# Optimization experiments

Measured on AMD Instinct MI355X. Metric: run time of the kernel, lower is better.

The kernel has to match this reference:

```python
import jax, jax.numpy as jnp
import numpy as np

B = 512       # number of graphs
MAX_N = 128   # pad length (>= max(num_atoms))
D = 256       # emb_dim


def setup_inputs() -> dict:
    key = jax.random.key(0)
    ks = jax.random.split(key, 20)
    num_atoms_np = np.full(B, 80, dtype=np.int64)
    num_atoms_np[: B // 2] = 112
    num_atoms_np[B // 2 :] = 48
    total = int(num_atoms_np.sum())  # 40960, static
    scale = 1.0 / np.sqrt(D)

    def lin_w(k):
        return jax.random.normal(k, (D, D), jnp.float32) * scale

    inp = {
        'rep_2d': jax.random.normal(ks[0], (total, D), jnp.float32),
        'rep_3d': jax.random.normal(ks[1], (total, D), jnp.float32),
        'num_atoms': jnp.asarray(num_atoms_np),
        # mha_2d_3d (queries from 2d, keys/values from 3d)
        'wq23': lin_w(ks[2]), 'bq23': jnp.zeros((D,), jnp.float32),
        'wk23': lin_w(ks[3]), 'bk23': jnp.zeros((D,), jnp.float32),
        'wv23': lin_w(ks[4]), 'bv23': jnp.zeros((D,), jnp.float32),
        # mha_3d_2d (queries from 3d, keys/values from 2d)
        'wq32': lin_w(ks[5]), 'bq32': jnp.zeros((D,), jnp.float32),
        'wk32': lin_w(ks[6]), 'bk32': jnp.zeros((D,), jnp.float32),
        'wv32': lin_w(ks[7]), 'bv32': jnp.zeros((D,), jnp.float32),
        # per-branch Linear (normalizer=Identity) + GELU
        'wm23': lin_w(ks[8]), 'bm23': jnp.zeros((D,), jnp.float32),
        'wm32': lin_w(ks[9]), 'bm32': jnp.zeros((D,), jnp.float32),
    }
    return inp


def _variadic_to_padded(flat, num_atoms):
    # flat: [total, D] -> padded [B, MAX_N, D], mask [B, MAX_N] (True = valid)
    cum = jnp.cumsum(num_atoms)
    offsets = cum - num_atoms
    pos = jnp.arange(MAX_N)
    mask = pos[None, :] < num_atoms[:, None]
    idx = jnp.where(mask, offsets[:, None] + pos[None, :], 0)
    padded = flat[idx] * mask[..., None].astype(flat.dtype)
    return padded, mask


def _padded_to_variadic(padded, num_atoms, total):
    # padded: [B, MAX_N, D] -> flat [total, D]
    cum = jnp.cumsum(num_atoms)
    t = jnp.arange(total)
    b = jnp.searchsorted(cum, t, side='right')
    i = t - (cum - num_atoms)[b]
    return padded[b, i]


def _cross_attn(q_in, kv_in, mask, wq, bq, wk, bk, wv, bv):
    # single-head scaled dot-product cross-attention, key-side padding mask
    q = q_in @ wq.T + bq
    k = kv_in @ wk.T + bk
    v = kv_in @ wv.T + bv
    s = jnp.einsum('bqd,bkd->bqk', q, k) / jnp.sqrt(jnp.asarray(D, q.dtype))
    s = jnp.where(mask[:, None, :], s, jnp.asarray(-1e9, s.dtype))
    a = jax.nn.softmax(s, axis=-1)
    return jnp.einsum('bqk,bkd->bqd', a, v)


def reference(rep_2d, rep_3d, num_atoms,
              wq23, bq23, wk23, bk23, wv23, bv23,
              wq32, bq32, wk32, bk32, wv32, bv32,
              wm23, bm23, wm32, bm32):
    total = rep_2d.shape[0]
    p2d, mask = _variadic_to_padded(rep_2d, num_atoms)
    p3d, _ = _variadic_to_padded(rep_3d, num_atoms)
    x2d = _cross_attn(p2d, p3d, mask, wq23, bq23, wk23, bk23, wv23, bv23)
    x3d = _cross_attn(p3d, p2d, mask, wq32, bq32, wk32, bk32, wv32, bv32)
    x2d = _padded_to_variadic(x2d, num_atoms, total)
    x3d = _padded_to_variadic(x3d, num_atoms, total)
    out2d = jax.nn.gelu(x2d @ wm23.T + bm23, approximate=False)
    out3d = jax.nn.gelu(x3d @ wm32.T + bm32, approximate=False)
    return (out2d, out3d)
```

## Files before the change

### kernel.cpp

```cpp
#include <hip/hip_runtime.h>
#include <hip/hip_bf16.h>
#include <cstdint>


typedef short s16x8 __attribute__((ext_vector_type(8)));
typedef float f32x4 __attribute__((ext_vector_type(4)));

__device__ __forceinline__ s16x8 cvt8(const float* p) {
  float4 a0 = *(const float4*)p, a1 = *(const float4*)(p + 4);
  union { s16x8 v; __bf16 e[8]; } u;
  u.e[0] = (__bf16)a0.x; u.e[1] = (__bf16)a0.y; u.e[2] = (__bf16)a0.z; u.e[3] = (__bf16)a0.w;
  u.e[4] = (__bf16)a1.x; u.e[5] = (__bf16)a1.y; u.e[6] = (__bf16)a1.z; u.e[7] = (__bf16)a1.w;
  return u.v;
}
__device__ __forceinline__ float fast_gelu(float x) {
  float ax = fabsf(x);
  float t = 1.0f / (1.0f + 0.3275911f * (ax * 0.70710678f));
  float y = t * (0.254829592f + t * (-0.284496736f + t * (1.421413741f +
            t * (-1.453152027f + t * 1.061405429f))));
  float er = 1.0f - y * __expf(-0.5f * ax * ax);
  er = (x < 0.f) ? -er : er;
  return 0.5f * x * (1.0f + er);
}

__global__ void sentinel_kernel(float* out, float v) {
  if (threadIdx.x == 0 && blockIdx.x == 0) out[0] = v;
}

__global__ __launch_bounds__(512) void scan_kernel(
    const int* __restrict__ na, int* __restrict__ offs,
    int B, int total, float* out)
{
  __shared__ int s32[512];
  __shared__ int s64[512];
  const int t = threadIdx.x;
  int v32 = 0, v64 = 0;
  if (t < B) {
    v32 = na[t];
    v64 = (int)((const long long*)na)[t];
  }
  s32[t] = v32; s64[t] = v64;
  __syncthreads();
  for (int o = 1; o < 512; o <<= 1) {
    int a = (t >= o) ? s32[t - o] : 0;
    int b = (t >= o) ? s64[t - o] : 0;
    __syncthreads();
    s32[t] += a; s64[t] += b;
    __syncthreads();
  }
  int tot32 = s32[B - 1], tot64 = s64[B - 1];
  bool ok32 = (tot32 == total), ok64 = (tot64 == total);
  if (t < B) offs[t] = ok32 ? (s32[t] - v32) : ok64 ? (s64[t] - v64) : 0;
  if (t == 0) {
    offs[B] = ok32 ? tot32 : ok64 ? tot64 : 0;
    if (!ok32 && !ok64) out[0] = 31337.0f;
  }
}

__global__ __launch_bounds__(256) void cvt2_kernel(
    const float* __restrict__ in0, const float* __restrict__ in1,
    __bf16* __restrict__ out0, __bf16* __restrict__ out1) {
  const float* in = blockIdx.y ? in1 : in0;
  __bf16* out = blockIdx.y ? out1 : out0;
  int i = (blockIdx.x * 256 + threadIdx.x) * 4;
  float4 f = *(const float4*)(in + i);
  out[i + 0] = (__bf16)f.x; out[i + 1] = (__bf16)f.y;
  out[i + 2] = (__bf16)f.z; out[i + 3] = (__bf16)f.w;
}

__global__ __launch_bounds__(256) void gemm_kernel(
    const float* __restrict__ A, const float* __restrict__ Bw,
    const float* __restrict__ bias, __bf16* __restrict__ C, int N)
{
  __shared__ __bf16 At[128 * 32];
  __shared__ __bf16 Bt[128 * 32];
  const int t = threadIdx.x;
  const int lane = t & 63, w = t >> 6;
  const int wr = w >> 1, wc = w & 1;
  const int l15 = lane & 15, l4 = lane >> 4;
  const int by = blockIdx.x, bx = blockIdx.y;

  f32x4 acc[4][4];
  for (int m = 0; m < 4; ++m)
    for (int nn = 0; nn < 4; ++nn) acc[m][nn] = (f32x4){0.f, 0.f, 0.f, 0.f};

  for (int kk = 0; kk < 256; kk += 32) {
    for (int j = 0; j < 2; ++j) {
      int c = t + j * 256;
      int row = c >> 2, off0 = (c & 3) * 8;
      *(s16x8*)(&At[row * 32 + off0]) = cvt8(A + (size_t)(by * 128 + row) * 256 + kk + off0);
      *(s16x8*)(&Bt[row * 32 + off0]) = cvt8(Bw + (size_t)(bx * 128 + row) * 256 + kk + off0);
    }
    __syncthreads();
    s16x8 af[4], bfr[4];
    for (int m = 0; m < 4; ++m)
      af[m] = *(const s16x8*)(&At[(wr * 64 + m * 16 + l15) * 32 + l4 * 8]);
    for (int nn = 0; nn < 4; ++nn)
      bfr[nn] = *(const s16x8*)(&Bt[(wc * 64 + nn * 16 + l15) * 32 + l4 * 8]);
    for (int m = 0; m < 4; ++m)
      for (int nn = 0; nn < 4; ++nn)
        acc[m][nn] = __builtin_amdgcn_mfma_f32_16x16x32_bf16(af[m], bfr[nn], acc[m][nn], 0, 0, 0);
    __syncthreads();
  }

  for (int m = 0; m < 4; ++m) {
    int row0 = by * 128 + wr * 64 + m * 16 + l4 * 4;
    for (int nn = 0; nn < 4; ++nn) {
      int col = bx * 128 + wc * 64 + nn * 16 + l15;
      float bc = bias[col];
      for (int r = 0; r < 4; ++r) {
        int row = row0 + r;
        C[(size_t)row * N + col] = (__bf16)(acc[m][nn][r] + bc);
      }
    }
  }
}

#define CTP 136
__global__ __launch_bounds__(256) void vgemm_kernel(
    const float* __restrict__ A, const float* __restrict__ Bw,
    const float* __restrict__ bias, __bf16* __restrict__ Vt, int total)
{
  __shared__ __bf16 At[128 * 32];
  __shared__ __bf16 Bt[128 * 32];
  __shared__ __bf16 Ct[128 * CTP];
  const int t = threadIdx.x;
  const int lane = t & 63, w = t >> 6;
  const int wr = w >> 1, wc = w & 1;
  const int l15 = lane & 15, l4 = lane >> 4;
  const int by = blockIdx.x, bx = blockIdx.y;

  f32x4 acc[4][4];
  for (int m = 0; m < 4; ++m)
    for (int nn = 0; nn < 4; ++nn) acc[m][nn] = (f32x4){0.f, 0.f, 0.f, 0.f};

  for (int kk = 0; kk < 256; kk += 32) {
    for (int j = 0; j < 2; ++j) {
      int c = t + j * 256;
      int row = c >> 2, off0 = (c & 3) * 8;
      *(s16x8*)(&At[row * 32 + off0]) = cvt8(A + (size_t)(by * 128 + row) * 256 + kk + off0);
      *(s16x8*)(&Bt[row * 32 + off0]) = cvt8(Bw + (size_t)(bx * 128 + row) * 256 + kk + off0);
    }
    __syncthreads();
    s16x8 af[4], bfr[4];
    for (int m = 0; m < 4; ++m)
      af[m] = *(const s16x8*)(&At[(wr * 64 + m * 16 + l15) * 32 + l4 * 8]);
    for (int nn = 0; nn < 4; ++nn)
      bfr[nn] = *(const s16x8*)(&Bt[(wc * 64 + nn * 16 + l15) * 32 + l4 * 8]);
    for (int m = 0; m < 4; ++m)
      for (int nn = 0; nn < 4; ++nn)
        acc[m][nn] = __builtin_amdgcn_mfma_f32_16x16x32_bf16(af[m], bfr[nn], acc[m][nn], 0, 0, 0);
    __syncthreads();
  }

  for (int m = 0; m < 4; ++m) {
    int rl0 = wr * 64 + m * 16 + l4 * 4;
    for (int nn = 0; nn < 4; ++nn) {
      int cl = wc * 64 + nn * 16 + l15;
      for (int r = 0; r < 4; ++r) {
        int rl = rl0 + r;
        Ct[rl * CTP + cl] = (__bf16)(acc[m][nn][r] + bias[by * 128 + rl]);
      }
    }
  }
  __syncthreads();

  for (int i = 0; i < 8; ++i) {
    int c = t + i * 256;
    int row = c >> 4, seg = c & 15;
    *(uint4*)(Vt + (size_t)(by * 128 + row) * total + bx * 128 + seg * 8) =
        *(const uint4*)(&Ct[row * CTP + seg * 8]);
  }
}

struct Attn2Args {
  const __bf16* Q[2]; const __bf16* K[2]; const __bf16* V[2];
  unsigned long long X[2];
};
#define KP 264
#define PP 136
#define XP 272
__global__ __launch_bounds__(512, 2) void attn2_kernel(
    Attn2Args args, const int* __restrict__ offs, int total)
{
  __shared__ __bf16 smem[128 * 136];
  __bf16 (*Klds)[KP] = (__bf16(*)[KP])smem;
  __bf16 (*Plds)[PP] = (__bf16(*)[PP])smem;
  __bf16 (*XT)[XP]   = (__bf16(*)[XP])smem;

  const int br = blockIdx.y;
  const __bf16* Q  = args.Q[br];
  const __bf16* Km = args.K[br];
  const __bf16* Vt = args.V[br];
  __bf16* X = (__bf16*)args.X[br];

  const int g = blockIdx.x;
  const int off = offs[g];
  const int n = offs[g + 1] - off;
  const int t = threadIdx.x, lane = t & 63, w = t >> 6;
  const int l15 = lane & 15, l4 = lane >> 4;
  const bool qact = (w * 16) < n;
  const bool big = (n > 64);

  const int srow = t >> 5, scol = (t & 31) * 16;
  uint4 kst[4];
  #pragma unroll
  for (int j = 0; j < 4; ++j)
    kst[j] = *(const uint4*)((const char*)(Km + (size_t)(off + j * 16 + srow) * 256) + scol);
  s16x8 qf[8];
  if (qact) {
    int qr = w * 16 + l15; if (qr >= n) qr = n - 1;
    const __bf16* qp = Q + (size_t)(off + qr) * 256 + l4 * 8;
    #pragma unroll
    for (int kk = 0; kk < 8; ++kk) qf[kk] = *(const s16x8*)(qp + kk * 32);
  }
  #pragma unroll
  for (int j = 0; j < 4; ++j)
    *(uint4*)((char*)&Klds[j * 16 + srow][0] + scol) = kst[j];
  uint4 kst1[4];
  if (big) {
    #pragma unroll
    for (int j = 0; j < 4; ++j)
      kst1[j] = *(const uint4*)((const char*)(Km + (size_t)(off + 64 + j * 16 + srow) * 256) + scol);
  }
  __syncthreads();

  f32x4 sacc[8];
  #pragma unroll
  for (int i = 0; i < 8; ++i) sacc[i] = (f32x4){0.f, 0.f, 0.f, 0.f};
  if (qact) {
    #pragma unroll
    for (int kt = 0; kt < 4; ++kt) {
      const __bf16* kp = &Klds[kt * 16 + l15][l4 * 8];
      #pragma unroll
      for (int kk = 0; kk < 8; ++kk) {
        s16x8 kf = *(const s16x8*)(kp + kk * 32);
        sacc[kt] = __builtin_amdgcn_mfma_f32_16x16x32_bf16(qf[kk], kf, sacc[kt], 0, 0, 0);
      }
    }
  }
  __syncthreads();
  if (big) {
    #pragma unroll
    for (int j = 0; j < 4; ++j)
      *(uint4*)((char*)&Klds[j * 16 + srow][0] + scol) = kst1[j];
    __syncthreads();
    if (qact) {
      #pragma unroll
      for (int kt = 0; kt < 4; ++kt) {
        const __bf16* kp = &Klds[kt * 16 + l15][l4 * 8];
        #pragma unroll
        for (int kk = 0; kk < 8; ++kk) {
          s16x8 kf = *(const s16x8*)(kp + kk * 32);
          sacc[4 + kt] = __builtin_amdgcn_mfma_f32_16x16x32_bf16(qf[kk], kf, sacc[4 + kt], 0, 0, 0);
        }
      }
    }
    __syncthreads();
  }

  if (qact) {
    #pragma unroll
    for (int r = 0; r < 4; ++r) {
      float sv[8];
      float m = -1e30f;
      #pragma unroll
      for (int kt = 0; kt < 8; ++kt) {
        int key = kt * 16 + l15;
        float v = (key < n) ? sacc[kt][r] * 0.0625f : -1e30f;
        sv[kt] = v; m = fmaxf(m, v);
      }
      for (int o = 1; o < 16; o <<= 1) m = fmaxf(m, __shfl_xor(m, o));
      float p[8], sum = 0.f;
      #pragma unroll
      for (int kt = 0; kt < 8; ++kt) { p[kt] = __expf(sv[kt] - m); sum += p[kt]; }
      for (int o = 1; o < 16; o <<= 1) sum += __shfl_xor(sum, o);
      float inv = 1.f / sum;
      int q = w * 16 + l4 * 4 + r;
      #pragma unroll
      for (int kt = 0; kt < 4; ++kt)
        Plds[q][kt * 16 + l15] = (__bf16)(p[kt] * inv);
      if (big) {
        #pragma unroll
        for (int kt = 4; kt < 8; ++kt)
          Plds[q][kt * 16 + l15] = (__bf16)(p[kt] * inv);
      }
    }
  }
  __syncthreads();

  const int dbase = w * 32;
  f32x4 xacc[2][8];
  #pragma unroll
  for (int dt = 0; dt < 2; ++dt)
    #pragma unroll
    for (int qm = 0; qm < 8; ++qm) xacc[dt][qm] = (f32x4){0.f, 0.f, 0.f, 0.f};

  #pragma unroll
  for (int dt = 0; dt < 2; ++dt) {
    int d = dbase + dt * 16 + l15;
    s16x8 vf[4];
    #pragma unroll
    for (int ks = 0; ks < 4; ++ks) {
      int kc = off + ks * 32 + l4 * 8;
      if (kc > total - 8) kc = total - 8;
      vf[ks] = *(const s16x8*)(Vt + (size_t)d * total + kc);
    }
    #pragma unroll
    for (int qm = 0; qm < 8; ++qm) {
      #pragma unroll
      for (int ks = 0; ks < 4; ++ks) {
        if (ks * 32 < n) {
          s16x8 pa = *(const s16x8*)(&Plds[qm * 16 + l15][ks * 32 + l4 * 8]);
          xacc[dt][qm] = __builtin_amdgcn_mfma_f32_16x16x32_bf16(pa, vf[ks], xacc[dt][qm], 0, 0, 0);
        }
      }
    }
  }
  __syncthreads();

  #pragma unroll
  for (int dt = 0; dt < 2; ++dt)
    #pragma unroll
    for (int qm = 0; qm < 4; ++qm)
      #pragma unroll
      for (int r = 0; r < 4; ++r)
        XT[qm * 16 + l4 * 4 + r][dbase + dt * 16 + l15] = (__bf16)xacc[dt][qm][r];
  __syncthreads();
  #pragma unroll
  for (int i = 0; i < 4; ++i) {
    int c = t + i * 512;
    int row = c >> 5, seg = c & 31;
    if (row < n)
      *(uint4*)(X + (size_t)(off + row) * 256 + seg * 8) =
          *(const uint4*)(&XT[row][seg * 8]);
  }
  if (big) {
    __syncthreads();
    #pragma unroll
    for (int dt = 0; dt < 2; ++dt)
      #pragma unroll
      for (int qm = 4; qm < 8; ++qm)
        #pragma unroll
        for (int r = 0; r < 4; ++r)
          XT[(qm - 4) * 16 + l4 * 4 + r][dbase + dt * 16 + l15] = (__bf16)xacc[dt][qm][r];
    __syncthreads();
    #pragma unroll
    for (int i = 0; i < 4; ++i) {
      int c = t + i * 512;
      int row = c >> 5, seg = c & 31;
      int grow = 64 + row;
      if (grow < n)
        *(uint4*)(X + (size_t)(off + grow) * 256 + seg * 8) =
            *(const uint4*)(&XT[row][seg * 8]);
    }
  }
}

__global__ __launch_bounds__(256) void gemm_out(
    const __bf16* __restrict__ A, const __bf16* __restrict__ W,
    const float* __restrict__ bias, float* __restrict__ C)
{
  __shared__ __bf16 At[64 * 32];
  __shared__ __bf16 Bt[128 * 32];
  const int t = threadIdx.x;
  const int lane = t & 63, w = t >> 6;
  const int wr = w >> 1, wc = w & 1;
  const int l15 = lane & 15, l4 = lane >> 4;
  const int by = blockIdx.x, bx = blockIdx.y;

  f32x4 acc[2][4];
  for (int m = 0; m < 2; ++m)
    for (int nn = 0; nn < 4; ++nn) acc[m][nn] = (f32x4){0.f, 0.f, 0.f, 0.f};

  for (int kk = 0; kk < 256; kk += 32) {
    {
      int row = t >> 2, off0 = (t & 3) * 8;
      *(s16x8*)(&At[row * 32 + off0]) =
          *(const s16x8*)(A + (size_t)(by * 64 + row) * 256 + kk + off0);
    }
    for (int j = 0; j < 2; ++j) {
      int c = t + j * 256;
      int row = c >> 2, off0 = (c & 3) * 8;
      *(s16x8*)(&Bt[row * 32 + off0]) =
          *(const s16x8*)(W + (size_t)(bx * 128 + row) * 256 + kk + off0);
    }
    __syncthreads();
    s16x8 af[2], bfr[4];
    for (int m = 0; m < 2; ++m)
      af[m] = *(const s16x8*)(&At[(wr * 32 + m * 16 + l15) * 32 + l4 * 8]);
    for (int nn = 0; nn < 4; ++nn)
      bfr[nn] = *(const s16x8*)(&Bt[(wc * 64 + nn * 16 + l15) * 32 + l4 * 8]);
    for (int m = 0; m < 2; ++m)
      for (int nn = 0; nn < 4; ++nn)
        acc[m][nn] = __builtin_amdgcn_mfma_f32_16x16x32_bf16(af[m], bfr[nn], acc[m][nn], 0, 0, 0);
    __syncthreads();
  }

  for (int m = 0; m < 2; ++m) {
    int row0 = by * 64 + wr * 32 + m * 16 + l4 * 4;
    for (int nn = 0; nn < 4; ++nn) {
      int col = bx * 128 + wc * 64 + nn * 16 + l15;
      float bc = bias[col];
      for (int r = 0; r < 4; ++r) {
        int row = row0 + r;
        C[(size_t)row * 256 + col] = fast_gelu(acc[m][nn][r] + bc);
      }
    }
  }
}

extern "C" void kernel_launch(void* const* d_in, const int* in_sizes, int n_in,
                              void* d_out, int out_size, void* d_ws, size_t ws_size,
                              hipStream_t stream) {
  const float* rep2d = (const float*)d_in[0];
  const float* rep3d = (const float*)d_in[1];
  const int*   na    = (const int*)d_in[2];
  const float* wq23 = (const float*)d_in[3];  const float* bq23 = (const float*)d_in[4];
  const float* wk23 = (const float*)d_in[5];  const float* bk23 = (const float*)d_in[6];
  const float* wv23 = (const float*)d_in[7];  const float* bv23 = (const float*)d_in[8];
  const float* wq32 = (const float*)d_in[9];  const float* bq32 = (const float*)d_in[10];
  const float* wk32 = (const float*)d_in[11]; const float* bk32 = (const float*)d_in[12];
  const float* wv32 = (const float*)d_in[13]; const float* bv32 = (const float*)d_in[14];
  const float* wm23 = (const float*)d_in[15]; const float* bm23 = (const float*)d_in[16];
  const float* wm32 = (const float*)d_in[17]; const float* bm32 = (const float*)d_in[18];

  const int B = in_sizes[2];
  const int total = in_sizes[0] / 256;
  float* out = (float*)d_out;

  char* ws = (char*)d_ws;
  const size_t SZ = (size_t)total * 256 * sizeof(__bf16);
  const size_t WMB = 65536 * sizeof(__bf16);
  const size_t need6 = 8192 + 2 * WMB + 6 * SZ;
  const size_t need3 = 8192 + 2 * WMB + 3 * SZ;
  int* offs = (int*)ws;

  dim3 blk(256);
  dim3 blkA(512);
  dim3 gP(total / 128, 2);
  dim3 gV(2, total / 128);
  dim3 gO(total / 64, 2);

  if (ws_size >= need6) {
    __bf16* WM0 = (__bf16*)(ws + 8192);
    __bf16* WM1 = (__bf16*)(ws + 8192 + WMB);
    __bf16* BQ1 = (__bf16*)(ws + 8192 + 2 * WMB);
    __bf16* BK1 = (__bf16*)(ws + 8192 + 2 * WMB + SZ);
    __bf16* BV1 = (__bf16*)(ws + 8192 + 2 * WMB + 2 * SZ);
    __bf16* BQ2 = (__bf16*)(ws + 8192 + 2 * WMB + 3 * SZ);
    __bf16* BK2 = (__bf16*)(ws + 8192 + 2 * WMB + 4 * SZ);
    __bf16* BV2 = (__bf16*)(ws + 8192 + 2 * WMB + 5 * SZ);

    scan_kernel<<<1, 512, 0, stream>>>(na, offs, B, total, out);
    cvt2_kernel<<<dim3(64, 2), blk, 0, stream>>>(wm23, wm32, WM0, WM1);
    gemm_kernel<<<gP, blk, 0, stream>>>(rep2d, wq23, bq23, BQ1, 256);
    gemm_kernel<<<gP, blk, 0, stream>>>(rep3d, wk23, bk23, BK1, 256);
    vgemm_kernel<<<gV, blk, 0, stream>>>(wv23, rep3d, bv23, BV1, total);
    gemm_kernel<<<gP, blk, 0, stream>>>(rep3d, wq32, bq32, BQ2, 256);
    gemm_kernel<<<gP, blk, 0, stream>>>(rep2d, wk32, bk32, BK2, 256);
    vgemm_kernel<<<gV, blk, 0, stream>>>(wv32, rep2d, bv32, BV2, total);

    Attn2Args aa;
    aa.Q[0] = BQ1; aa.K[0] = BK1; aa.V[0] = BV1; aa.X[0] = (unsigned long long)BQ1;
    aa.Q[1] = BQ2; aa.K[1] = BK2; aa.V[1] = BV2; aa.X[1] = (unsigned long long)BQ2;
    attn2_kernel<<<dim3(B, 2), blkA, 0, stream>>>(aa, offs, total);

    gemm_out<<<gO, blk, 0, stream>>>(BQ1, WM0, bm23, out);
    gemm_out<<<gO, blk, 0, stream>>>(BQ2, WM1, bm32, out + (size_t)total * 256);
  } else if (ws_size >= need3) {
    __bf16* WM0 = (__bf16*)(ws + 8192);
    __bf16* WM1 = (__bf16*)(ws + 8192 + WMB);
    __bf16* BQ = (__bf16*)(ws + 8192 + 2 * WMB);
    __bf16* BK = (__bf16*)(ws + 8192 + 2 * WMB + SZ);
    __bf16* BV = (__bf16*)(ws + 8192 + 2 * WMB + 2 * SZ);

    scan_kernel<<<1, 512, 0, stream>>>(na, offs, B, total, out);
    cvt2_kernel<<<dim3(64, 2), blk, 0, stream>>>(wm23, wm32, WM0, WM1);
    for (int br = 0; br < 2; ++br) {
      const float* rq = br ? rep3d : rep2d;
      const float* rk = br ? rep2d : rep3d;
      const float* wq = br ? wq32 : wq23;  const float* bq = br ? bq32 : bq23;
      const float* wk = br ? wk32 : wk23;  const float* bk = br ? bk32 : bk23;
      const float* wv = br ? wv32 : wv23;  const float* bv = br ? bv32 : bv23;
      __bf16* wm = br ? WM1 : WM0;         const float* bm = br ? bm32 : bm23;
      float* o = out + (size_t)br * total * 256;

      gemm_kernel<<<gP, blk, 0, stream>>>(rq, wq, bq, BQ, 256);
      gemm_kernel<<<gP, blk, 0, stream>>>(rk, wk, bk, BK, 256);
      vgemm_kernel<<<gV, blk, 0, stream>>>(wv, rk, bv, BV, total);
      Attn2Args aa;
      aa.Q[0] = BQ; aa.K[0] = BK; aa.V[0] = BV; aa.X[0] = (unsigned long long)BQ;
      aa.Q[1] = BQ; aa.K[1] = BK; aa.V[1] = BV; aa.X[1] = (unsigned long long)BQ;
      attn2_kernel<<<dim3(B, 1), blkA, 0, stream>>>(aa, offs, total);
      gemm_out<<<gO, blk, 0, stream>>>(BQ, wm, bm, o);
    }
  } else {
    sentinel_kernel<<<1, 64, 0, stream>>>(out, 54321.0f);
  }
}
```

Before: 214.6 us.

## Tile-major V layout for coalesced attention loads; wider padded K tile in output GEMM

The V-projection kernel now writes Vt in a 16x16 tile-major layout, so the attention kernel's P·V fragment loads become contiguous 512-byte blocks instead of strided rows of a d-major matrix. Separately, the output GEMM stages 64-wide K slices into padded LDS (stride 88) and runs two MFMA sub-steps per barrier, halving the number of sync iterations and reducing bank conflicts. The changes add index arithmetic and more LDS use, and they rely on total being a multiple of 16.

```diff
diff --git a/kernel.cpp b/kernel.cpp
--- a/kernel.cpp
+++ b/kernel.cpp
@@ -167,9 +167,11 @@
 
   for (int i = 0; i < 8; ++i) {
     int c = t + i * 256;
-    int row = c >> 4, seg = c & 15;
-    *(uint4*)(Vt + (size_t)(by * 128 + row) * total + bx * 128 + seg * 8) =
-        *(const uint4*)(&Ct[row * CTP + seg * 8]);
+    int tile = c >> 5, w5 = c & 31;
+    int kb_l = tile >> 3, db_l = tile & 7;
+    int d_l = w5 & 15, kh = w5 >> 4;
+    *(uint4*)(Vt + (((size_t)(bx * 8 + kb_l) * 16 + (by * 8 + db_l)) << 8) + w5 * 8) =
+        *(const uint4*)(&Ct[(db_l * 16 + d_l) * CTP + kb_l * 16 + kh * 8]);
   }
 }
 
@@ -290,6 +292,7 @@
   __syncthreads();
 
   const int dbase = w * 32;
+  const int ktiles = total >> 4;
   f32x4 xacc[2][8];
   #pragma unroll
   for (int dt = 0; dt < 2; ++dt)
@@ -298,13 +301,14 @@
 
   #pragma unroll
   for (int dt = 0; dt < 2; ++dt) {
-    int d = dbase + dt * 16 + l15;
+    int db = w * 2 + dt;
     s16x8 vf[4];
     #pragma unroll
     for (int ks = 0; ks < 4; ++ks) {
-      int kc = off + ks * 32 + l4 * 8;
-      if (kc > total - 8) kc = total - 8;
-      vf[ks] = *(const s16x8*)(Vt + (size_t)d * total + kc);
+      int kb = (off >> 4) + ks * 2 + (l4 >> 1);
+      if (kb >= ktiles) kb = ktiles - 1;
+      vf[ks] = *(const s16x8*)(Vt + (((size_t)kb * 16 + db) << 8)
+                               + (l15 + ((l4 & 1) << 4)) * 8);
     }
     #pragma unroll
     for (int qm = 0; qm < 8; ++qm) {
@@ -357,12 +361,13 @@
   }
 }
 
+#define OP 88
 __global__ __launch_bounds__(256) void gemm_out(
     const __bf16* __restrict__ A, const __bf16* __restrict__ W,
     const float* __restrict__ bias, float* __restrict__ C)
 {
-  __shared__ __bf16 At[64 * 32];
-  __shared__ __bf16 Bt[128 * 32];
+  __shared__ __bf16 At[64 * OP];
+  __shared__ __bf16 Bt[128 * OP];
   const int t = threadIdx.x;
   const int lane = t & 63, w = t >> 6;
   const int wr = w >> 1, wc = w & 1;
@@ -373,27 +378,37 @@
   for (int m = 0; m < 2; ++m)
     for (int nn = 0; nn < 4; ++nn) acc[m][nn] = (f32x4){0.f, 0.f, 0.f, 0.f};
 
-  for (int kk = 0; kk < 256; kk += 32) {
-    {
-      int row = t >> 2, off0 = (t & 3) * 8;
-      *(s16x8*)(&At[row * 32 + off0]) =
-          *(const s16x8*)(A + (size_t)(by * 64 + row) * 256 + kk + off0);
-    }
+  for (int kk = 0; kk < 256; kk += 64) {
+    #pragma unroll
     for (int j = 0; j < 2; ++j) {
       int c = t + j * 256;
-      int row = c >> 2, off0 = (c & 3) * 8;
-      *(s16x8*)(&Bt[row * 32 + off0]) =
+      int row = c >> 3, off0 = (c & 7) * 8;
+      *(s16x8*)(&At[row * OP + off0]) =
+          *(const s16x8*)(A + (size_t)(by * 64 + row) * 256 + kk + off0);
+    }
+    #pragma unroll
+    for (int j = 0; j < 4; ++j) {
+      int c = t + j * 256;
+      int row = c >> 3, off0 = (c & 7) * 8;
+      *(s16x8*)(&Bt[row * OP + off0]) =
           *(const s16x8*)(W + (size_t)(bx * 128 + row) * 256 + kk + off0);
     }
     __syncthreads();
-    s16x8 af[2], bfr[4];
-    for (int m = 0; m < 2; ++m)
-      af[m] = *(const s16x8*)(&At[(wr * 32 + m * 16 + l15) * 32 + l4 * 8]);
-    for (int nn = 0; nn < 4; ++nn)
-      bfr[nn] = *(const s16x8*)(&Bt[(wc * 64 + nn * 16 + l15) * 32 + l4 * 8]);
-    for (int m = 0; m < 2; ++m)
+    #pragma unroll
+    for (int k2 = 0; k2 < 2; ++k2) {
+      s16x8 af[2], bfr[4];
+      #pragma unroll
+      for (int m = 0; m < 2; ++m)
+        af[m] = *(const s16x8*)(&At[(wr * 32 + m * 16 + l15) * OP + k2 * 32 + l4 * 8]);
+      #pragma unroll
       for (int nn = 0; nn < 4; ++nn)
-        acc[m][nn] = __builtin_amdgcn_mfma_f32_16x16x32_bf16(af[m], bfr[nn], acc[m][nn], 0, 0, 0);
+        bfr[nn] = *(const s16x8*)(&Bt[(wc * 64 + nn * 16 + l15) * OP + k2 * 32 + l4 * 8]);
+      #pragma unroll
+      for (int m = 0; m < 2; ++m)
+        #pragma unroll
+        for (int nn = 0; nn < 4; ++nn)
+          acc[m][nn] = __builtin_amdgcn_mfma_f32_16x16x32_bf16(af[m], bfr[nn], acc[m][nn], 0, 0, 0);
+    }
     __syncthreads();
   }
 
```

Result: faster. 204.9 us (-4.5%).
